# Kernel tuning notes

Measured on AMD Instinct MI355X. Metric: run time of the kernel, lower is better.

The kernel has to match this reference:

```python
import jax, jax.numpy as jnp
import numpy as np

B, L, D, H = 2, 2048, 1024, 16
DK = D // H

def setup_inputs() -> dict:
    key = jax.random.key(0)
    ks = jax.random.split(key, 3)
    x = jax.random.normal(ks[0], (B, L, D), dtype=jnp.float32)
    w_qkv = jax.random.normal(ks[1], (D, 3 * D), dtype=jnp.float32) * 0.02
    b_qkv = jnp.zeros((3 * D,), dtype=jnp.float32)
    w_o = jax.random.normal(ks[2], (D, D), dtype=jnp.float32) * 0.02
    b_o = jnp.zeros((D,), dtype=jnp.float32)
    # causal additive mask [1,1,L,L]: 0 on/below diagonal, -1e9 above
    causal = jnp.tril(jnp.ones((L, L), dtype=bool))
    mask = jnp.where(causal, 0.0, -1e9).astype(jnp.float32)[None, None]
    return {"x": x, "w_qkv": w_qkv, "b_qkv": b_qkv, "w_o": w_o, "b_o": b_o, "mask": mask}

def _split_heads(t):
    b, l, _ = t.shape
    return t.reshape(b, l, H, DK).transpose(0, 2, 1, 3)  # [B,H,L,DK]

def reference(x, w_qkv, b_qkv, w_o, b_o, mask):
    qkv = x @ w_qkv + b_qkv                     # [B,L,3D]
    q, k, v = jnp.split(qkv, 3, axis=-1)
    q, k, v = _split_heads(q), _split_heads(k), _split_heads(v)
    scale = 1.0 / np.sqrt(DK).astype(np.float32)
    scores = jnp.einsum('bhld,bhmd->bhlm', q, k) * scale + mask  # [B,H,L,L]
    attn = jax.nn.softmax(scores, axis=-1)
    ctx = jnp.einsum('bhlm,bhmd->bhld', attn, v)  # [B,H,L,DK]
    ctx = ctx.transpose(0, 2, 1, 3).reshape(x.shape[0], x.shape[1], D)
    out = ctx @ w_o + b_o  # dropout is identity in eval mode
    return out, k, v  # (output, new_cache k, new_cache v)
```

## Files before the change

kernel.cpp:

```cpp
#include <hip/hip_runtime.h>
#include <hip/hip_bf16.h>
#include <stdint.h>

typedef __hip_bfloat16 bf16;
typedef __attribute__((ext_vector_type(8))) short short8;
typedef __attribute__((ext_vector_type(4))) float f32x4;

#define DEVFN static __device__ __forceinline__

DEVFN unsigned short f2bf(float f) {
    bf16 h = __float2bfloat16(f);
    return __builtin_bit_cast(unsigned short, h);
}

DEVFN void gload_lds16(const void* g, void* l) {
    __builtin_amdgcn_global_load_lds((const __attribute__((address_space(1))) void*)g,
                                     (__attribute__((address_space(3))) void*)l, 16, 0, 0);
}


__global__ void cvt_x_kernel(const float* __restrict__ in, bf16* __restrict__ out) {
    int i = blockIdx.x * 256 + threadIdx.x;
    float4 v = ((const float4*)in)[i];
    ushort4 o;
    o.x = f2bf(v.x); o.y = f2bf(v.y); o.z = f2bf(v.z); o.w = f2bf(v.w);
    ((ushort4*)out)[i] = o;
}

__global__ void transpose_cvt_kernel(const float* __restrict__ in, bf16* __restrict__ out,
                                     int R, int C) {
    __shared__ float tile[32][33];
    int c0 = blockIdx.x * 32, r0 = blockIdx.y * 32;
    int tx = threadIdx.x, ty = threadIdx.y;
    #pragma unroll
    for (int i = 0; i < 4; ++i)
        tile[ty + i * 8][tx] = in[(long)(r0 + ty + i * 8) * C + c0 + tx];
    __syncthreads();
    #pragma unroll
    for (int i = 0; i < 4; ++i)
        out[(long)(c0 + ty + i * 8) * R + r0 + tx] = __float2bfloat16(tile[tx][ty + i * 8]);
}

__global__ __launch_bounds__(256) void vt_kernel(const unsigned short* __restrict__ v,
                                                 unsigned short* __restrict__ vt) {
    __shared__ unsigned short tile[64][66];
    const int bh = blockIdx.y;
    const int kc0 = blockIdx.x * 64;
    const int t = threadIdx.x;
    const int c = t & 63, r4 = t >> 6;
    const unsigned short* src = v + ((long)bh * 2048 + kc0) * 64;
    #pragma unroll
    for (int i = 0; i < 16; ++i) {
        int row = r4 * 16 + i;
        tile[row][c] = src[row * 64 + c];
    }
    __syncthreads();
    unsigned short* dst = vt + (long)bh * 64 * 2048 + kc0;
    #pragma unroll
    for (int i = 0; i < 16; ++i) {
        int d = r4 * 16 + i;
        dst[(long)d * 2048 + c] = tile[c][d];
    }
}


template <int EPI>
__global__ __launch_bounds__(256) void gemm_kernel(
    const bf16* __restrict__ A, const bf16* __restrict__ BT, const float* __restrict__ bias,
    float* __restrict__ o_k, float* __restrict__ o_v,
    bf16* __restrict__ qws, bf16* __restrict__ kws, bf16* __restrict__ vws,
    float* __restrict__ outp)
{
    __shared__ bf16 lsA[128 * 32];
    __shared__ bf16 lsB[128 * 32];
    const int t = threadIdx.x;
    const int l = t & 63, w = t >> 6;
    const int lr = l & 15, lg = l >> 4;
    const int bx = blockIdx.x, by = blockIdx.y;
    const int wr = w >> 1, wc = w & 1;

    f32x4 acc[4][4] = {};

    const bf16* gA = A + ((long)by * 128 + (t >> 2)) * 1024 + (t & 3) * 8;
    const bf16* gB = BT + ((long)bx * 128 + (t >> 2)) * 1024 + (t & 3) * 8;
    char* lA = (char*)lsA + w * 1024;
    char* lB = (char*)lsB + w * 1024;

    for (int k0 = 0; k0 < 1024; k0 += 32) {
        __syncthreads();
        gload_lds16(gA + k0,         lA);
        gload_lds16(gA + k0 + 65536, lA + 4096);
        gload_lds16(gB + k0,         lB);
        gload_lds16(gB + k0 + 65536, lB + 4096);
        __syncthreads();

        short8 af[4], bfr[4];
        #pragma unroll
        for (int i = 0; i < 4; ++i)
            af[i] = *(const short8*)((const char*)lsA + (wr * 64 + i * 16 + lr) * 64 + lg * 16);
        #pragma unroll
        for (int j = 0; j < 4; ++j)
            bfr[j] = *(const short8*)((const char*)lsB + (wc * 64 + j * 16 + lr) * 64 + lg * 16);
        #pragma unroll
        for (int i = 0; i < 4; ++i)
            #pragma unroll
            for (int j = 0; j < 4; ++j)
                acc[i][j] = __builtin_amdgcn_mfma_f32_16x16x32_bf16(af[i], bfr[j], acc[i][j], 0, 0, 0);
    }

    const int m0 = by * 128 + wr * 64;
    const int n0 = bx * 128 + wc * 64;
    #pragma unroll
    for (int j = 0; j < 4; ++j) {
        const int cg = n0 + j * 16 + lr;
        const float bv = bias[cg];
        if constexpr (EPI == 0) {
            const int part = cg >> 10, cc = cg & 1023;
            const int h = cc >> 6, dk = cc & 63;
            #pragma unroll
            for (int i = 0; i < 4; ++i) {
                #pragma unroll
                for (int r = 0; r < 4; ++r) {
                    const int rg = m0 + i * 16 + lg * 4 + r;
                    const int bb = rg >> 11, li = rg & 2047;
                    const float v = acc[i][j][r] + bv;
                    const int idx = ((bb * 16 + h) * 2048 + li) * 64 + dk;
                    if (part == 0) {
                        qws[idx] = __float2bfloat16(v * 0.125f);
                    } else if (part == 1) {
                        o_k[idx] = v; kws[idx] = __float2bfloat16(v);
                    } else {
                        o_v[idx] = v; vws[idx] = __float2bfloat16(v);
                    }
                }
            }
        } else {
            #pragma unroll
            for (int i = 0; i < 4; ++i)
                #pragma unroll
                for (int r = 0; r < 4; ++r) {
                    const int rg = m0 + i * 16 + lg * 4 + r;
                    outp[(long)rg * 1024 + cg] = acc[i][j][r] + bv;
                }
        }
    }
}


__global__ __launch_bounds__(256) void attn_kernel(
    const bf16* __restrict__ qws, const bf16* __restrict__ kws,
    const bf16* __restrict__ vtws, bf16* __restrict__ ctx)
{
    const int bh = blockIdx.x;
    const int qt = 31 - (int)blockIdx.y;
    const int qb = qt * 64;
    const int t = threadIdx.x;
    const int l = t & 63, w = t >> 6;
    const int lr = l & 15, lg = l >> 4;

    __shared__ bf16 Kt[2][64 * 64];
    __shared__ bf16 Vt[2][64 * 64];
    __shared__ bf16 Pt[4][16 * 64];

    const char* Kg = (const char*)(kws + (long)bh * 2048 * 64);
    const char* Vg = (const char*)(vtws + (long)bh * 64 * 2048);

    const int srow0 = t >> 3;
    const int scoff = ((t & 7) * 16) ^ ((srow0 & 7) << 4);

    auto STAGE = [&](int buf, int kv) {
        #pragma unroll
        for (int r = 0; r < 2; ++r) {
            int row = r * 32 + srow0;
            char* ldsbase_k = (char*)Kt[buf] + r * 4096 + w * 1024;
            char* ldsbase_v = (char*)Vt[buf] + r * 4096 + w * 1024;
            gload_lds16(Kg + (long)(kv + row) * 128 + scoff, ldsbase_k);
            gload_lds16(Vg + (long)row * 4096 + (long)kv * 2 + scoff, ldsbase_v);
        }
    };

    const bf16* Qg = qws + (long)bh * 2048 * 64;
    short8 qf[2];
    #pragma unroll
    for (int kk = 0; kk < 2; ++kk)
        qf[kk] = *(const short8*)(Qg + (qb + w * 16 + lr) * 64 + kk * 32 + lg * 8);

    f32x4 acc[4] = {};
    float mrun = -1e30f;
    float lsum = 0.f;
    const int kvend = qb + 64;

    STAGE(0, 0);
    __syncthreads();
    int cur = 0;

    for (int kv = 0; kv < kvend; kv += 64) {
        if (kv + 64 < kvend) STAGE(cur ^ 1, kv + 64);

        f32x4 st[4];
        #pragma unroll
        for (int tt = 0; tt < 4; ++tt) {
            int row = tt * 16 + lr;
            short8 kf0 = *(const short8*)((const char*)Kt[cur] + row * 128 + ((lg * 16) ^ ((row & 7) << 4)));
            short8 kf1 = *(const short8*)((const char*)Kt[cur] + row * 128 + ((64 + lg * 16) ^ ((row & 7) << 4)));
            f32x4 sa = {};
            sa = __builtin_amdgcn_mfma_f32_16x16x32_bf16(kf0, qf[0], sa, 0, 0, 0);
            sa = __builtin_amdgcn_mfma_f32_16x16x32_bf16(kf1, qf[1], sa, 0, 0, 0);
            st[tt] = sa;
        }

        if (kv + 64 > qb) {
            int qr = qb + w * 16 + lr;
            #pragma unroll
            for (int tt = 0; tt < 4; ++tt)
                #pragma unroll
                for (int r = 0; r < 4; ++r) {
                    int kc = kv + tt * 16 + lg * 4 + r;
                    if (kc > qr) st[tt][r] = -1e30f;
                }
        }

        {
            float mx = -1e30f;
            #pragma unroll
            for (int tt = 0; tt < 4; ++tt)
                #pragma unroll
                for (int r = 0; r < 4; ++r) mx = fmaxf(mx, st[tt][r]);
            mx = fmaxf(mx, __shfl_xor(mx, 16));
            mx = fmaxf(mx, __shfl_xor(mx, 32));
            float mnew = fmaxf(mrun, mx);
            float corr = __expf(mrun - mnew);
            float ts = 0.f;
            #pragma unroll
            for (int tt = 0; tt < 4; ++tt) {
                float p0 = __expf(st[tt][0] - mnew);
                float p1 = __expf(st[tt][1] - mnew);
                float p2 = __expf(st[tt][2] - mnew);
                float p3 = __expf(st[tt][3] - mnew);
                ts += (p0 + p1) + (p2 + p3);
                ushort4 pb;
                pb.x = f2bf(p0); pb.y = f2bf(p1); pb.z = f2bf(p2); pb.w = f2bf(p3);
                int row = lr;
                *(ushort4*)((char*)Pt[w] + row * 128 + ((tt * 32 + lg * 8) ^ ((row & 7) << 4))) = pb;
            }
            ts += __shfl_xor(ts, 16);
            ts += __shfl_xor(ts, 32);
            lsum = lsum * corr + ts;
            mrun = mnew;
            float cb0 = __shfl(corr, lg * 4 + 0);
            float cb1 = __shfl(corr, lg * 4 + 1);
            float cb2 = __shfl(corr, lg * 4 + 2);
            float cb3 = __shfl(corr, lg * 4 + 3);
            #pragma unroll
            for (int j = 0; j < 4; ++j) {
                acc[j][0] *= cb0; acc[j][1] *= cb1;
                acc[j][2] *= cb2; acc[j][3] *= cb3;
            }
        }

        #pragma unroll
        for (int kk = 0; kk < 2; ++kk) {
            int row = lr;
            short8 pa = *(const short8*)((const char*)Pt[w] + row * 128 + ((kk * 64 + lg * 16) ^ ((row & 7) << 4)));
            #pragma unroll
            for (int j = 0; j < 4; ++j) {
                int dv = j * 16 + lr;
                short8 vb = *(const short8*)((const char*)Vt[cur] + dv * 128 + ((kk * 64 + lg * 16) ^ ((dv & 7) << 4)));
                acc[j] = __builtin_amdgcn_mfma_f32_16x16x32_bf16(pa, vb, acc[j], 0, 0, 0);
            }
        }

        __syncthreads();
        cur ^= 1;
    }

    const int b = bh >> 4, h = bh & 15;
    {
        float i0 = 1.f / __shfl(lsum, lg * 4 + 0);
        float i1 = 1.f / __shfl(lsum, lg * 4 + 1);
        float i2 = 1.f / __shfl(lsum, lg * 4 + 2);
        float i3 = 1.f / __shfl(lsum, lg * 4 + 3);
        #pragma unroll
        for (int j = 0; j < 4; ++j) {
            int dv = j * 16 + lr;
            int qr0 = qb + w * 16 + lg * 4;
            long base = ((long)(b * 2048 + qr0)) * 1024 + h * 64 + dv;
            ctx[base]            = __float2bfloat16(acc[j][0] * i0);
            ctx[base + 1024]     = __float2bfloat16(acc[j][1] * i1);
            ctx[base + 2048]     = __float2bfloat16(acc[j][2] * i2);
            ctx[base + 3072]     = __float2bfloat16(acc[j][3] * i3);
        }
    }
}


extern "C" void kernel_launch(void* const* d_in, const int* in_sizes, int n_in,
                              void* d_out, int out_size, void* d_ws, size_t ws_size,
                              hipStream_t stream) {
    (void)in_sizes; (void)n_in; (void)out_size; (void)ws_size;
    const float* x     = (const float*)d_in[0];
    const float* w_qkv = (const float*)d_in[1];
    const float* b_qkv = (const float*)d_in[2];
    const float* w_o   = (const float*)d_in[3];
    const float* b_o   = (const float*)d_in[4];

    float* out = (float*)d_out;
    float* o_k = out + 4194304;
    float* o_v = o_k + 4194304;

    char* ws = (char*)d_ws;
    bf16* xbf   = (bf16*)(ws);
    bf16* wqkvT = (bf16*)(ws + (8u  << 20));
    bf16* woT   = (bf16*)(ws + (14u << 20));
    bf16* qws   = (bf16*)(ws + (16u << 20));
    bf16* kws   = (bf16*)(ws + (24u << 20));
    bf16* vws   = (bf16*)(ws + (32u << 20));
    bf16* ctx   = (bf16*)(ws + (40u << 20));
    bf16* vtws  = xbf;

    cvt_x_kernel<<<4096, 256, 0, stream>>>(x, xbf);
    transpose_cvt_kernel<<<dim3(96, 32), dim3(32, 8), 0, stream>>>(w_qkv, wqkvT, 1024, 3072);
    transpose_cvt_kernel<<<dim3(32, 32), dim3(32, 8), 0, stream>>>(w_o, woT, 1024, 1024);
    gemm_kernel<0><<<dim3(24, 32), 256, 0, stream>>>(xbf, wqkvT, b_qkv, o_k, o_v,
                                                     qws, kws, vws, nullptr);
    vt_kernel<<<dim3(32, 32), 256, 0, stream>>>((const unsigned short*)vws,
                                                (unsigned short*)vtws);
    attn_kernel<<<dim3(32, 32), 256, 0, stream>>>(qws, kws, vtws, ctx);
    gemm_kernel<1><<<dim3(8, 32), 256, 0, stream>>>(ctx, woT, b_o, nullptr, nullptr,
                                                    nullptr, nullptr, nullptr, out);
}
```

Baseline: 221.7 us.

## Merge prep kernels, use exp2 softmax with folded log2e, add MFMA priority hints

Merges the x conversion and both weight transpose-convert kernels into a single launch, which saves two kernel launches. Folds log2(e) into the Q scale so the softmax can use the native exp2 instruction instead of __expf. Defers the row-sum cross-lane shuffles until after the KV loop and flattens the max reduction into a tree. Wraps the MFMA sections in s_setprio hints so they get issue priority. The exp2 rewrite relies on the mask being applied as -1e30 after scaling, which it is.

```diff
diff --git a/kernel.cpp b/kernel.cpp
--- a/kernel.cpp
+++ b/kernel.cpp
@@ -13,25 +13,42 @@
     return __builtin_bit_cast(unsigned short, h);
 }
 
+DEVFN float exp2fast(float x) {
+    return __builtin_amdgcn_exp2f(x);
+}
+
 DEVFN void gload_lds16(const void* g, void* l) {
     __builtin_amdgcn_global_load_lds((const __attribute__((address_space(1))) void*)g,
                                      (__attribute__((address_space(3))) void*)l, 16, 0, 0);
 }
 
 
-__global__ void cvt_x_kernel(const float* __restrict__ in, bf16* __restrict__ out) {
-    int i = blockIdx.x * 256 + threadIdx.x;
-    float4 v = ((const float4*)in)[i];
-    ushort4 o;
-    o.x = f2bf(v.x); o.y = f2bf(v.y); o.z = f2bf(v.z); o.w = f2bf(v.w);
-    ((ushort4*)out)[i] = o;
-}
-
-__global__ void transpose_cvt_kernel(const float* __restrict__ in, bf16* __restrict__ out,
-                                     int R, int C) {
+__global__ __launch_bounds__(256) void prep_kernel(
+    const float* __restrict__ x, bf16* __restrict__ xbf,
+    const float* __restrict__ wq, bf16* __restrict__ wqT,
+    const float* __restrict__ wo, bf16* __restrict__ woT)
+{
     __shared__ float tile[32][33];
-    int c0 = blockIdx.x * 32, r0 = blockIdx.y * 32;
-    int tx = threadIdx.x, ty = threadIdx.y;
+    const int bid = blockIdx.x;
+    const int t = threadIdx.x;
+    if (bid < 4096) {
+        int i = bid * 256 + t;
+        float4 v = ((const float4*)x)[i];
+        ushort4 o;
+        o.x = f2bf(v.x); o.y = f2bf(v.y); o.z = f2bf(v.z); o.w = f2bf(v.w);
+        ((ushort4*)xbf)[i] = o;
+        return;
+    }
+    const float* in; bf16* out; int R, C, bx, by;
+    if (bid < 4096 + 3072) {
+        int b = bid - 4096; bx = b % 96; by = b / 96;
+        in = wq; out = wqT; R = 1024; C = 3072;
+    } else {
+        int b = bid - 7168; bx = b & 31; by = b >> 5;
+        in = wo; out = woT; R = 1024; C = 1024;
+    }
+    int c0 = bx * 32, r0 = by * 32;
+    int tx = t & 31, ty = t >> 5;
     #pragma unroll
     for (int i = 0; i < 4; ++i)
         tile[ty + i * 8][tx] = in[(long)(r0 + ty + i * 8) * C + c0 + tx];
@@ -126,7 +143,7 @@
                     const float v = acc[i][j][r] + bv;
                     const int idx = ((bb * 16 + h) * 2048 + li) * 64 + dk;
                     if (part == 0) {
-                        qws[idx] = __float2bfloat16(v * 0.125f);
+                        qws[idx] = __float2bfloat16(v * 0.18033688011112042f);
                     } else if (part == 1) {
                         o_k[idx] = v; kws[idx] = __float2bfloat16(v);
                     } else {
@@ -198,6 +215,7 @@
         if (kv + 64 < kvend) STAGE(cur ^ 1, kv + 64);
 
         f32x4 st[4];
+        __builtin_amdgcn_s_setprio(1);
         #pragma unroll
         for (int tt = 0; tt < 4; ++tt) {
             int row = tt * 16 + lr;
@@ -208,6 +226,7 @@
             sa = __builtin_amdgcn_mfma_f32_16x16x32_bf16(kf1, qf[1], sa, 0, 0, 0);
             st[tt] = sa;
         }
+        __builtin_amdgcn_s_setprio(0);
 
         if (kv + 64 > qb) {
             int qr = qb + w * 16 + lr;
@@ -221,30 +240,28 @@
         }
 
         {
-            float mx = -1e30f;
-            #pragma unroll
-            for (int tt = 0; tt < 4; ++tt)
-                #pragma unroll
-                for (int r = 0; r < 4; ++r) mx = fmaxf(mx, st[tt][r]);
+            float v0 = fmaxf(fmaxf(st[0][0], st[1][0]), fmaxf(st[2][0], st[3][0]));
+            float v1 = fmaxf(fmaxf(st[0][1], st[1][1]), fmaxf(st[2][1], st[3][1]));
+            float v2 = fmaxf(fmaxf(st[0][2], st[1][2]), fmaxf(st[2][2], st[3][2]));
+            float v3 = fmaxf(fmaxf(st[0][3], st[1][3]), fmaxf(st[2][3], st[3][3]));
+            float mx = fmaxf(fmaxf(v0, v1), fmaxf(v2, v3));
             mx = fmaxf(mx, __shfl_xor(mx, 16));
             mx = fmaxf(mx, __shfl_xor(mx, 32));
             float mnew = fmaxf(mrun, mx);
-            float corr = __expf(mrun - mnew);
+            float corr = exp2fast(mrun - mnew);
             float ts = 0.f;
             #pragma unroll
             for (int tt = 0; tt < 4; ++tt) {
-                float p0 = __expf(st[tt][0] - mnew);
-                float p1 = __expf(st[tt][1] - mnew);
-                float p2 = __expf(st[tt][2] - mnew);
-                float p3 = __expf(st[tt][3] - mnew);
+                float p0 = exp2fast(st[tt][0] - mnew);
+                float p1 = exp2fast(st[tt][1] - mnew);
+                float p2 = exp2fast(st[tt][2] - mnew);
+                float p3 = exp2fast(st[tt][3] - mnew);
                 ts += (p0 + p1) + (p2 + p3);
                 ushort4 pb;
                 pb.x = f2bf(p0); pb.y = f2bf(p1); pb.z = f2bf(p2); pb.w = f2bf(p3);
                 int row = lr;
                 *(ushort4*)((char*)Pt[w] + row * 128 + ((tt * 32 + lg * 8) ^ ((row & 7) << 4))) = pb;
             }
-            ts += __shfl_xor(ts, 16);
-            ts += __shfl_xor(ts, 32);
             lsum = lsum * corr + ts;
             mrun = mnew;
             float cb0 = __shfl(corr, lg * 4 + 0);
@@ -258,6 +275,7 @@
             }
         }
 
+        __builtin_amdgcn_s_setprio(1);
         #pragma unroll
         for (int kk = 0; kk < 2; ++kk) {
             int row = lr;
@@ -269,10 +287,14 @@
                 acc[j] = __builtin_amdgcn_mfma_f32_16x16x32_bf16(pa, vb, acc[j], 0, 0, 0);
             }
         }
+        __builtin_amdgcn_s_setprio(0);
 
         __syncthreads();
         cur ^= 1;
     }
+
+    lsum += __shfl_xor(lsum, 16);
+    lsum += __shfl_xor(lsum, 32);
 
     const int b = bh >> 4, h = bh & 15;
     {
@@ -318,9 +340,7 @@
     bf16* ctx   = (bf16*)(ws + (40u << 20));
     bf16* vtws  = xbf;
 
-    cvt_x_kernel<<<4096, 256, 0, stream>>>(x, xbf);
-    transpose_cvt_kernel<<<dim3(96, 32), dim3(32, 8), 0, stream>>>(w_qkv, wqkvT, 1024, 3072);
-    transpose_cvt_kernel<<<dim3(32, 32), dim3(32, 8), 0, stream>>>(w_o, woT, 1024, 1024);
+    prep_kernel<<<8192, 256, 0, stream>>>(x, xbf, w_qkv, wqkvT, w_o, woT);
     gemm_kernel<0><<<dim3(24, 32), 256, 0, stream>>>(xbf, wqkvT, b_qkv, o_k, o_v,
                                                      qws, kws, vws, nullptr);
     vt_kernel<<<dim3(32, 32), 256, 0, stream>>>((const unsigned short*)vws,
```

Result: no change. 218.1 us (-1.6%).
